# Kernel tuning notes

Hardware: AMD Instinct MI355X
Metric: run time of the kernel (lower is better)

Reference implementation:

```python
import jax, jax.numpy as jnp
import numpy as np

INPLANES = 768
HIDDEN = 64
NUM_EXPERTS = 6
TOP_K = 2


def setup_inputs() -> dict:
    key = jax.random.key(0)
    ks = jax.random.split(key, 7)
    B, C, D = 64, 320, INPLANES
    x = jax.random.normal(ks[0], (B, C, D), dtype=jnp.float32)
    xi = jax.random.normal(ks[1], (B, C, D), dtype=jnp.float32)
    # gating network: per-token logits over experts
    w_gate = jax.random.normal(ks[2], (D, NUM_EXPERTS), dtype=jnp.float32) / np.sqrt(D)
    # LoRA-style experts: down-projection D -> HIDDEN per expert
    expert_w = jax.random.normal(ks[3], (NUM_EXPERTS, D, HIDDEN), dtype=jnp.float32) / np.sqrt(D)
    expert_b = jnp.zeros((NUM_EXPERTS, HIDDEN), dtype=jnp.float32)
    # reprojection ffn1_1: Linear(HIDDEN, INPLANES), torch convention W:[out,in]
    ffn1_w = jax.random.normal(ks[4], (D, HIDDEN), dtype=jnp.float32) / np.sqrt(HIDDEN)
    ffn1_b = jnp.zeros((D,), dtype=jnp.float32)
    return {"x": x, "xi": xi, "w_gate": w_gate, "expert_w": expert_w,
            "expert_b": expert_b, "ffn1_w": ffn1_w, "ffn1_b": ffn1_b}


def _cv_squared(v):
    eps = 1e-10
    return jnp.var(v) / (jnp.mean(v) ** 2 + eps)


def reference(x, xi, w_gate, expert_w, expert_b, ffn1_w, ffn1_b):
    B, C, D = x.shape
    nz = C // 5
    # slice template (z) and search (x) token streams from both modalities
    z0, x0 = x[:, :nz, :], x[:, nz:, :]
    z1, x1 = xi[:, :nz, :], xi[:, nz:, :]
    # MoE_lora: fuse the two modalities and route tokens (z tokens first, then x)
    inp = jnp.concatenate([z0 + z1, x0 + x1], axis=1)        # [B, C, D]
    tok = inp.reshape(-1, D)                                  # [N, D], N = B*C
    N = tok.shape[0]
    # noisy-top-k gating (clean/eval path): top-2 experts, softmax over kept logits
    logits = tok @ w_gate                                     # [N, E]
    top_vals, top_idx = jax.lax.top_k(logits, TOP_K)          # [N, k]
    top_gates = jax.nn.softmax(top_vals, axis=-1)             # [N, k]
    gates = jnp.zeros_like(logits).at[jnp.arange(N)[:, None], top_idx].add(top_gates)
    # expert LoRA down-projections, combined by sparse gates (dense-equivalent math)
    h = jnp.einsum('nd,edh->enh', tok, expert_w) + expert_b[:, None, :]  # [E, N, H]
    y = jnp.einsum('ne,enh->nh', gates, h)                    # [N, H]
    y = y.reshape(B, C, HIDDEN)
    z_moe, x_moe = y[:, :nz, :], y[:, nz:, :]
    # load-balancing loss: cv^2 of importance + cv^2 of load
    importance = gates.sum(axis=0)
    load = (gates > 0).astype(jnp.float32).sum(axis=0)
    loss = _cv_squared(importance) + _cv_squared(load)
    # ffn1_1 reprojection back to inplanes
    x_prompted = x_moe @ ffn1_w.T + ffn1_b                    # [B, 4C/5, D]
    z_prompted = z_moe @ ffn1_w.T + ffn1_b                    # [B, C/5, D]
    return (x_prompted, z_prompted, loss, logits)
```

## Files before the change

### kernel.cpp

```cpp
#include <hip/hip_runtime.h>

typedef __attribute__((ext_vector_type(8))) short short8;
typedef __attribute__((ext_vector_type(4))) short short4v;
typedef __attribute__((ext_vector_type(4))) float f32x4;

#define VM(n) asm volatile("s_waitcnt vmcnt(" #n ")" ::: "memory")
#define LGKM0 asm volatile("s_waitcnt lgkmcnt(0)" ::: "memory")

namespace {

constexpr int DIN  = 768;
constexpr int HID  = 64;
constexpr int NEXP = 6;
constexpr int CDIM  = 320;
constexpr int NZ    = 64;
constexpr int NTOK  = 20480;

constexpr long long XP_OFF   = 0;
constexpr long long ZP_OFF   = 12582912LL;
constexpr long long LOSS_OFF = 15728640LL;
constexpr long long LG_OFF   = 15728641LL;

__device__ inline unsigned short f2bf(float f) {
  union { float f; unsigned u; } v{f};
  return (unsigned short)((v.u + 0x7FFFu + ((v.u >> 16) & 1u)) >> 16);
}
__device__ inline float b2f(unsigned short s) {
  union { unsigned u; float f; } v{(unsigned)s << 16};
  return v.f;
}
__device__ inline void gload16(const void* g, void* l) {
  __builtin_amdgcn_global_load_lds(
      (const __attribute__((address_space(1))) unsigned*)g,
      (__attribute__((address_space(3))) unsigned*)l, 16, 0, 0);
}
__device__ inline int row_base(int n) {
  int bb = n / CDIM, c = n - bb * CDIM;
  return (c < NZ) ? (int)(ZP_OFF + (long long)(bb * NZ + c) * DIN)
                  : (int)(XP_OFF + (long long)(bb * (CDIM - NZ) + (c - NZ)) * DIN);
}

__global__ __launch_bounds__(256) void pre_kernel(
    const float* __restrict__ x, const float* __restrict__ xi,
    const float* __restrict__ wg, const float* __restrict__ ew,
    const float* __restrict__ fw,
    float* __restrict__ out, float4* __restrict__ rec,
    unsigned short* __restrict__ ewb_t, unsigned short* __restrict__ fwb)
{
  int b = blockIdx.x, tid = threadIdx.x;
  __shared__ float t_lds[64][65];
  if (b < 72) {
    int e = b / 12, kc = (b % 12) * 64;
    const float* src = ew + (size_t)e * DIN * HID + (size_t)kc * HID;
    #pragma unroll
    for (int it = 0; it < 16; ++it) {
      int f = it * 256 + tid; int ky = f >> 6, h = f & 63;
      t_lds[h][ky] = src[ky * 64 + h];
    }
    __syncthreads();
    unsigned short* dst = ewb_t + (size_t)e * DIN * HID + kc;
    #pragma unroll
    for (int it = 0; it < 16; ++it) {
      int f = it * 256 + tid; int h = f >> 6, ky = f & 63;
      dst[(size_t)h * DIN + ky] = f2bf(t_lds[h][ky]);
    }
    return;
  }
  if (b < 84) {
    int base = (b - 72) * 4096;
    #pragma unroll
    for (int it = 0; it < 16; ++it) {
      int idx = base + it * 256 + tid;
      fwb[idx] = f2bf(fw[idx]);
    }
    return;
  }
  int wid = tid >> 6, lane = tid & 63;
  int n = (b - 84) * 4 + wid;
  float lg[NEXP];
  #pragma unroll
  for (int e = 0; e < NEXP; ++e) lg[e] = 0.f;

  const float4* xv  = reinterpret_cast<const float4*>(x  + (size_t)n * DIN);
  const float4* xiv = reinterpret_cast<const float4*>(xi + (size_t)n * DIN);
  unsigned short* tk = (unsigned short*)out + (size_t)row_base(n) * 2;
  #pragma unroll
  for (int j = 0; j < 3; ++j) {
    int f = lane + 64 * j;
    float4 a = xv[f], bq = xiv[f];
    float t0 = a.x + bq.x, t1 = a.y + bq.y, t2 = a.z + bq.z, t3 = a.w + bq.w;
    short4v tv;
    tv[0] = (short)f2bf(t0); tv[1] = (short)f2bf(t1);
    tv[2] = (short)f2bf(t2); tv[3] = (short)f2bf(t3);
    *(short4v*)(tk + f * 4) = tv;
    int d = f * 4;
    #pragma unroll
    for (int e = 0; e < NEXP; ++e) {
      lg[e] += t0 * wg[(d + 0) * NEXP + e] + t1 * wg[(d + 1) * NEXP + e]
             + t2 * wg[(d + 2) * NEXP + e] + t3 * wg[(d + 3) * NEXP + e];
    }
  }
  #pragma unroll
  for (int e = 0; e < NEXP; ++e) {
    float v = lg[e];
    #pragma unroll
    for (int off = 32; off >= 1; off >>= 1) v += __shfl_xor(v, off, 64);
    lg[e] = v;
  }
  int e0 = 0; float v0 = lg[0];
  #pragma unroll
  for (int j = 1; j < NEXP; ++j) if (lg[j] > v0) { v0 = lg[j]; e0 = j; }
  int e1 = 0; float v1 = -3.4e38f;
  #pragma unroll
  for (int j = 0; j < NEXP; ++j) if (j != e0 && lg[j] > v1) { v1 = lg[j]; e1 = j; }
  float g0 = 1.f / (1.f + expf(v1 - v0));
  if (lane < NEXP) {
    float myv = lg[0];
    #pragma unroll
    for (int e = 1; e < NEXP; ++e) if (lane == e) myv = lg[e];
    out[LG_OFF + (size_t)n * NEXP + lane] = myv;
  }
  if (lane == 0) rec[n] = make_float4((float)e0, (float)e1, g0, 1.f - g0);
}

__global__ __launch_bounds__(512) void moe_kernel(
    const unsigned short* __restrict__ ewb_t, const float* __restrict__ eb,
    const unsigned short* __restrict__ fwb, const float* __restrict__ fb,
    const float4* __restrict__ rec, float* __restrict__ out)
{
  __shared__ __align__(16) char smem[74752];
  __shared__ int rb[64];
  __shared__ float simp[8][NEXP], sld[8][NEXP];

  int tid = threadIdx.x, lane = tid & 63, wid = tid >> 6;
  int qw = lane >> 4, l15 = lane & 15;
  int wm = wid >> 2, wn = wid & 3;

  if (blockIdx.x == 320) {
    float imp[NEXP], ld[NEXP];
    #pragma unroll
    for (int e = 0; e < NEXP; ++e) { imp[e] = 0.f; ld[e] = 0.f; }
    for (int n = tid; n < NTOK; n += 512) {
      float4 r = rec[n];
      int e0 = (int)r.x, e1 = (int)r.y;
      #pragma unroll
      for (int e = 0; e < NEXP; ++e) {
        imp[e] += (e == e0 ? r.z : 0.f) + (e == e1 ? r.w : 0.f);
        ld[e]  += (e == e0 ? 1.f : 0.f) + (e == e1 ? 1.f : 0.f);
      }
    }
    #pragma unroll
    for (int e = 0; e < NEXP; ++e) {
      float a = imp[e], bq = ld[e];
      #pragma unroll
      for (int off = 32; off >= 1; off >>= 1) {
        a += __shfl_xor(a, off, 64);
        bq += __shfl_xor(bq, off, 64);
      }
      imp[e] = a; ld[e] = bq;
    }
    if (lane == 0) {
      #pragma unroll
      for (int e = 0; e < NEXP; ++e) { simp[wid][e] = imp[e]; sld[wid][e] = ld[e]; }
    }
    __syncthreads();
    if (tid == 0) {
      float It[NEXP], Lt[NEXP], mi = 0.f, ml = 0.f;
      #pragma unroll
      for (int e = 0; e < NEXP; ++e) {
        It[e] = 0.f; Lt[e] = 0.f;
        #pragma unroll
        for (int w = 0; w < 8; ++w) { It[e] += simp[w][e]; Lt[e] += sld[w][e]; }
        mi += It[e]; ml += Lt[e];
      }
      mi /= NEXP; ml /= NEXP;
      float vi = 0.f, vl = 0.f;
      #pragma unroll
      for (int e = 0; e < NEXP; ++e) {
        vi += (It[e] - mi) * (It[e] - mi);
        vl += (Lt[e] - ml) * (Lt[e] - ml);
      }
      vi /= NEXP; vl /= NEXP;
      out[LOSS_OFF] = vi / (mi * mi + 1e-10f) + vl / (ml * ml + 1e-10f);
    }
    return;
  }

  int t0 = blockIdx.x * 64;
  const unsigned short* tokb = (const unsigned short*)out;

  size_t b_src[3]; int b_dst[3];
  #pragma unroll
  for (int it = 0; it < 3; ++it) {
    int F = it * 512 + tid, r = F >> 2, s = F & 3;
    b_src[it] = (size_t)r * DIN + ((s ^ (r & 3) ^ ((r & 4) >> 1)) << 3);
    b_dst[it] = (it * 512 + wid * 64) * 16;
  }
  int ar = tid >> 2, as = tid & 3;
  size_t a_src = (size_t)row_base(t0 + ar) * 2 +
                 ((as ^ (ar & 3) ^ ((ar & 4) >> 1)) << 3);
  int a_dst = (wid * 64) * 16;

  if (tid < 64) rb[tid] = row_base(t0 + tid);

  #pragma unroll
  for (int it = 0; it < 3; ++it)
    gload16(ewb_t + b_src[it], smem + 8192 + b_dst[it]);
  if (tid < 256) gload16(tokb + a_src, smem + a_dst);

  f32x4 acc[2][6];
  #pragma unroll
  for (int m = 0; m < 2; ++m)
    #pragma unroll
    for (int n = 0; n < 6; ++n) acc[m][n] = (f32x4){0.f, 0.f, 0.f, 0.f};

  int aoff[2], boff[6];
  #pragma unroll
  for (int m = 0; m < 2; ++m) {
    int row = wm * 32 + m * 16 + l15;
    aoff[m] = row * 64 + ((qw ^ (row & 3) ^ ((row & 4) >> 1)) << 4);
  }
  #pragma unroll
  for (int n = 0; n < 6; ++n) {
    int row = wn * 96 + n * 16 + l15;
    boff[n] = row * 64 + ((qw ^ (row & 3) ^ ((row & 4) >> 1)) << 4);
  }

  for (int k = 0; k < 24; ++k) {
    const char* cA = smem + (k & 1) * 4096;
    const char* cB = smem + 8192 + (k & 1) * 24576;
    char* nA = (char*)smem + ((k + 1) & 1) * 4096;
    char* nB = (char*)smem + 8192 + ((k + 1) & 1) * 24576;
    if (k < 23) {
      #pragma unroll
      for (int it = 0; it < 3; ++it)
        gload16(ewb_t + b_src[it] + (k + 1) * 32, nB + b_dst[it]);
      if (tid < 256) gload16(tokb + a_src + (k + 1) * 32, nA + a_dst);
      if (wid < 4) VM(4); else VM(3);
    } else {
      VM(0);
    }
    __builtin_amdgcn_s_barrier();
    __builtin_amdgcn_sched_barrier(0);
    short8 af[2], bfv[6];
    #pragma unroll
    for (int m = 0; m < 2; ++m) af[m] = *(const short8*)(cA + aoff[m]);
    #pragma unroll
    for (int n = 0; n < 6; ++n) bfv[n] = *(const short8*)(cB + boff[n]);
    __builtin_amdgcn_s_setprio(1);
    #pragma unroll
    for (int m = 0; m < 2; ++m)
      #pragma unroll
      for (int n = 0; n < 6; ++n)
        acc[m][n] = __builtin_amdgcn_mfma_f32_16x16x32_bf16(af[m], bfv[n], acc[m][n], 0, 0, 0);
    __builtin_amdgcn_s_setprio(0);
    __builtin_amdgcn_sched_barrier(0);
    __builtin_amdgcn_s_barrier();
  }

  #pragma unroll
  for (int it = 0; it < 2; ++it) {
    int F = it * 512 + tid, r = F >> 3, s = F & 7;
    gload16(fwb + (size_t)r * HID + ((s ^ (r & 7)) << 3),
            smem + 58368 + (it * 512 + wid * 64) * 16);
  }

  unsigned short* hl = (unsigned short*)(smem + 8192);
  #pragma unroll
  for (int m = 0; m < 2; ++m)
    #pragma unroll
    for (int n = 0; n < 6; ++n)
      #pragma unroll
      for (int i = 0; i < 4; ++i) {
        int row = wm * 32 + m * 16 + qw * 4 + i;
        int col = wn * 96 + n * 16 + l15;
        hl[row * 392 + col] = f2bf(acc[m][n][i]);
      }
  LGKM0;
  __builtin_amdgcn_s_barrier();

  {
    int t = tid >> 3, j0 = (tid & 7) * 8;
    float4 rr = rec[t0 + t];
    int e0 = (int)rr.x, e1 = (int)rr.y;
    float g0 = rr.z, g1 = rr.w;
    short8 h0 = *(const short8*)(hl + t * 392 + e0 * 64 + j0);
    short8 h1 = *(const short8*)(hl + t * 392 + e1 * 64 + j0);
    const float4* ep0 = (const float4*)(eb + e0 * 64 + j0);
    const float4* ep1 = (const float4*)(eb + e1 * 64 + j0);
    float4 b0a = ep0[0], b0b = ep0[1], b1a = ep1[0], b1b = ep1[1];
    float be0[8] = {b0a.x, b0a.y, b0a.z, b0a.w, b0b.x, b0b.y, b0b.z, b0b.w};
    float be1[8] = {b1a.x, b1a.y, b1a.z, b1a.w, b1b.x, b1b.y, b1b.z, b1b.w};
    short8 ov;
    #pragma unroll
    for (int j = 0; j < 8; ++j) {
      float v = g0 * (b2f((unsigned short)h0[j]) + be0[j])
              + g1 * (b2f((unsigned short)h1[j]) + be1[j]);
      ov[j] = (short)f2bf(v);
    }
    *(short8*)(smem + t * 128 + ((((tid & 7)) ^ (t & 7)) << 4)) = ov;
  }
  LGKM0;
  __builtin_amdgcn_s_barrier();

  for (int c = 0; c < 6; ++c) {
    const char* cF = smem + ((c & 1) ? 8192 : 58368);
    char* nF = (char*)smem + ((c & 1) ? 58368 : 8192);
    if (c < 5) {
      #pragma unroll
      for (int it = 0; it < 2; ++it) {
        int F = it * 512 + tid, r = F >> 3, s = F & 7;
        gload16(fwb + (size_t)((c + 1) * 128 + r) * HID + ((s ^ (r & 7)) << 3),
                nF + (it * 512 + wid * 64) * 16);
      }
      VM(2);
    } else {
      VM(0);
    }
    __builtin_amdgcn_s_barrier();
    __builtin_amdgcn_sched_barrier(0);
    f32x4 a2[2][2];
    #pragma unroll
    for (int m = 0; m < 2; ++m)
      #pragma unroll
      for (int n = 0; n < 2; ++n) a2[m][n] = (f32x4){0.f, 0.f, 0.f, 0.f};
    #pragma unroll
    for (int kk = 0; kk < 2; ++kk) {
      short8 ay[2], bw[2];
      #pragma unroll
      for (int m = 0; m < 2; ++m) {
        int row = wm * 32 + m * 16 + l15;
        ay[m] = *(const short8*)(smem + row * 128 + (((kk * 4 + qw) ^ (row & 7)) << 4));
      }
      #pragma unroll
      for (int n = 0; n < 2; ++n) {
        int rw = wn * 32 + n * 16 + l15;
        bw[n] = *(const short8*)(cF + rw * 128 + (((kk * 4 + qw) ^ (rw & 7)) << 4));
      }
      __builtin_amdgcn_s_setprio(1);
      #pragma unroll
      for (int m = 0; m < 2; ++m)
        #pragma unroll
        for (int n = 0; n < 2; ++n)
          a2[m][n] = __builtin_amdgcn_mfma_f32_16x16x32_bf16(ay[m], bw[n], a2[m][n], 0, 0, 0);
      __builtin_amdgcn_s_setprio(0);
    }
    #pragma unroll
    for (int n = 0; n < 2; ++n) {
      int col = c * 128 + wn * 32 + n * 16 + l15;
      float bias = fb[col];
      #pragma unroll
      for (int m = 0; m < 2; ++m)
        #pragma unroll
        for (int i = 0; i < 4; ++i) {
          int rl = wm * 32 + m * 16 + qw * 4 + i;
          out[(size_t)rb[rl] + col] = a2[m][n][i] + bias;
        }
    }
    __builtin_amdgcn_sched_barrier(0);
    __builtin_amdgcn_s_barrier();
  }
}

}

extern "C" void kernel_launch(void* const* d_in, const int* in_sizes, int n_in,
                              void* d_out, int out_size, void* d_ws, size_t ws_size,
                              hipStream_t stream)
{
  const float* x  = (const float*)d_in[0];
  const float* xi = (const float*)d_in[1];
  const float* wg = (const float*)d_in[2];
  const float* ew = (const float*)d_in[3];
  const float* eb = (const float*)d_in[4];
  const float* fw = (const float*)d_in[5];
  const float* fb = (const float*)d_in[6];
  float* out = (float*)d_out;

  char* w = (char*)d_ws;
  float4*         rec   = (float4*)w;
  unsigned short* ewb_t = (unsigned short*)(w + 327680);
  unsigned short* fwb   = (unsigned short*)(w + 327680 + 589824);

  pre_kernel<<<84 + NTOK / 4, 256, 0, stream>>>(x, xi, wg, ew, fw, out, rec, ewb_t, fwb);
  moe_kernel<<<321, 512, 0, stream>>>(ewb_t, eb, fwb, fb, rec, out);
}
```

Measured before the change: 69.83 us.

## Process one token per 8 lanes in gating pre-kernel with LDS-staged gate weights

```diff
diff --git a/kernel.cpp b/kernel.cpp
--- a/kernel.cpp
+++ b/kernel.cpp
@@ -48,8 +48,9 @@
     unsigned short* __restrict__ ewb_t, unsigned short* __restrict__ fwb)
 {
   int b = blockIdx.x, tid = threadIdx.x;
-  __shared__ float t_lds[64][65];
+  __shared__ __align__(16) char sbuf[18432];
   if (b < 72) {
+    float (*t_lds)[65] = (float(*)[65])sbuf;
     int e = b / 12, kc = (b % 12) * 64;
     const float* src = ew + (size_t)e * DIN * HID + (size_t)kc * HID;
     #pragma unroll
@@ -75,36 +76,52 @@
     }
     return;
   }
-  int wid = tid >> 6, lane = tid & 63;
-  int n = (b - 84) * 4 + wid;
+  float* wgl = (float*)sbuf;
+  {
+    const float4* src4 = (const float4*)wg;
+    float4* dst4 = (float4*)sbuf;
+    for (int i = tid; i < NEXP * DIN / 4; i += 256) dst4[i] = src4[i];
+  }
+  __syncthreads();
+
+  int lane = tid & 63, wid = tid >> 6;
+  int ls = lane & 7;
+  int n  = (b - 84) * 32 + wid * 8 + (lane >> 3);
+
+  const float4* xv  = reinterpret_cast<const float4*>(x  + (size_t)n * DIN);
+  const float4* iv  = reinterpret_cast<const float4*>(xi + (size_t)n * DIN);
+  unsigned short* tk = (unsigned short*)out + (size_t)row_base(n) * 2;
+
   float lg[NEXP];
   #pragma unroll
   for (int e = 0; e < NEXP; ++e) lg[e] = 0.f;
 
-  const float4* xv  = reinterpret_cast<const float4*>(x  + (size_t)n * DIN);
-  const float4* xiv = reinterpret_cast<const float4*>(xi + (size_t)n * DIN);
-  unsigned short* tk = (unsigned short*)out + (size_t)row_base(n) * 2;
-  #pragma unroll
-  for (int j = 0; j < 3; ++j) {
-    int f = lane + 64 * j;
-    float4 a = xv[f], bq = xiv[f];
-    float t0 = a.x + bq.x, t1 = a.y + bq.y, t2 = a.z + bq.z, t3 = a.w + bq.w;
-    short4v tv;
-    tv[0] = (short)f2bf(t0); tv[1] = (short)f2bf(t1);
-    tv[2] = (short)f2bf(t2); tv[3] = (short)f2bf(t3);
-    *(short4v*)(tk + f * 4) = tv;
-    int d = f * 4;
-    #pragma unroll
-    for (int e = 0; e < NEXP; ++e) {
-      lg[e] += t0 * wg[(d + 0) * NEXP + e] + t1 * wg[(d + 1) * NEXP + e]
-             + t2 * wg[(d + 2) * NEXP + e] + t3 * wg[(d + 3) * NEXP + e];
-    }
+  #pragma unroll 4
+  for (int k = 0; k < 24; ++k) {
+    float4 a = xv[ls + 8 * k];
+    float4 q = iv[ls + 8 * k];
+    float tv0 = a.x + q.x, tv1 = a.y + q.y, tv2 = a.z + q.z, tv3 = a.w + q.w;
+    short4v t4;
+    t4[0] = (short)f2bf(tv0); t4[1] = (short)f2bf(tv1);
+    t4[2] = (short)f2bf(tv2); t4[3] = (short)f2bf(tv3);
+    *(short4v*)(tk + ls * 4 + 32 * k) = t4;
+    const float4* wq = (const float4*)(wgl + ls * 24 + 192 * k);
+    float4 w0 = wq[0], w1 = wq[1], w2 = wq[2], w3 = wq[3], w4 = wq[4], w5 = wq[5];
+    lg[0] += tv0 * w0.x; lg[1] += tv0 * w0.y; lg[2] += tv0 * w0.z;
+    lg[3] += tv0 * w0.w; lg[4] += tv0 * w1.x; lg[5] += tv0 * w1.y;
+    lg[0] += tv1 * w1.z; lg[1] += tv1 * w1.w; lg[2] += tv1 * w2.x;
+    lg[3] += tv1 * w2.y; lg[4] += tv1 * w2.z; lg[5] += tv1 * w2.w;
+    lg[0] += tv2 * w3.x; lg[1] += tv2 * w3.y; lg[2] += tv2 * w3.z;
+    lg[3] += tv2 * w3.w; lg[4] += tv2 * w4.x; lg[5] += tv2 * w4.y;
+    lg[0] += tv3 * w4.z; lg[1] += tv3 * w4.w; lg[2] += tv3 * w5.x;
+    lg[3] += tv3 * w5.y; lg[4] += tv3 * w5.z; lg[5] += tv3 * w5.w;
   }
   #pragma unroll
   for (int e = 0; e < NEXP; ++e) {
     float v = lg[e];
-    #pragma unroll
-    for (int off = 32; off >= 1; off >>= 1) v += __shfl_xor(v, off, 64);
+    v += __shfl_xor(v, 1, 64);
+    v += __shfl_xor(v, 2, 64);
+    v += __shfl_xor(v, 4, 64);
     lg[e] = v;
   }
   int e0 = 0; float v0 = lg[0];
@@ -114,13 +131,13 @@
   #pragma unroll
   for (int j = 0; j < NEXP; ++j) if (j != e0 && lg[j] > v1) { v1 = lg[j]; e1 = j; }
   float g0 = 1.f / (1.f + expf(v1 - v0));
-  if (lane < NEXP) {
+  if (ls < NEXP) {
     float myv = lg[0];
     #pragma unroll
-    for (int e = 1; e < NEXP; ++e) if (lane == e) myv = lg[e];
-    out[LG_OFF + (size_t)n * NEXP + lane] = myv;
-  }
-  if (lane == 0) rec[n] = make_float4((float)e0, (float)e1, g0, 1.f - g0);
+    for (int e = 1; e < NEXP; ++e) if (ls == e) myv = lg[e];
+    out[LG_OFF + (size_t)n * NEXP + ls] = myv;
+  }
+  if (ls == 0) rec[n] = make_float4((float)e0, (float)e1, g0, 1.f - g0);
 }
 
 __global__ __launch_bounds__(512) void moe_kernel(
@@ -382,6 +399,6 @@
   unsigned short* ewb_t = (unsigned short*)(w + 327680);
   unsigned short* fwb   = (unsigned short*)(w + 327680 + 589824);
 
-  pre_kernel<<<84 + NTOK / 4, 256, 0, stream>>>(x, xi, wg, ew, fw, out, rec, ewb_t, fwb);
+  pre_kernel<<<84 + 640, 256, 0, stream>>>(x, xi, wg, ew, fw, out, rec, ewb_t, fwb);
   moe_kernel<<<321, 512, 0, stream>>>(ewb_t, eb, fwb, fb, rec, out);
 }
```

Result: no change. 68.69 us (-1.6%).

## Split weight prep into separate kernel and stage token rows via LDS

Applied to the files above, without the earlier changes.

```diff
diff --git a/kernel.cpp b/kernel.cpp
--- a/kernel.cpp
+++ b/kernel.cpp
@@ -40,12 +40,11 @@
                   : (int)(XP_OFF + (long long)(bb * (CDIM - NZ) + (c - NZ)) * DIN);
 }
 
-__global__ __launch_bounds__(256) void pre_kernel(
-    const float* __restrict__ x, const float* __restrict__ xi,
-    const float* __restrict__ wg, const float* __restrict__ ew,
-    const float* __restrict__ fw,
-    float* __restrict__ out, float4* __restrict__ rec,
-    unsigned short* __restrict__ ewb_t, unsigned short* __restrict__ fwb)
+__global__ __launch_bounds__(256) void prep_kernel(
+    const float* __restrict__ ew, const float* __restrict__ fw,
+    const float* __restrict__ wg,
+    unsigned short* __restrict__ ewb_t, unsigned short* __restrict__ fwb,
+    float* __restrict__ wgT)
 {
   int b = blockIdx.x, tid = threadIdx.x;
   __shared__ float t_lds[64][65];
@@ -64,40 +63,68 @@
       int f = it * 256 + tid; int h = f >> 6, ky = f & 63;
       dst[(size_t)h * DIN + ky] = f2bf(t_lds[h][ky]);
     }
-    return;
-  }
-  if (b < 84) {
+  } else if (b < 84) {
     int base = (b - 72) * 4096;
     #pragma unroll
     for (int it = 0; it < 16; ++it) {
       int idx = base + it * 256 + tid;
       fwb[idx] = f2bf(fw[idx]);
     }
-    return;
-  }
-  int wid = tid >> 6, lane = tid & 63;
-  int n = (b - 84) * 4 + wid;
+  } else {
+    for (int idx = tid; idx < NEXP * DIN; idx += 256) {
+      int e = idx / DIN, d = idx - e * DIN;
+      wgT[idx] = wg[d * NEXP + e];
+    }
+  }
+}
+
+__global__ __launch_bounds__(512) void pre_kernel(
+    const float* __restrict__ x, const float* __restrict__ xi,
+    const float* __restrict__ wgT_g,
+    float* __restrict__ out, float4* __restrict__ rec)
+{
+  __shared__ __align__(16) char sbuf[67584];
+  int tid = threadIdx.x, lane = tid & 63, w = tid >> 6;
+  int t0 = blockIdx.x * 8;
+  char* xl = sbuf;
+  char* il = sbuf + 24576;
+  const float* wgl = (const float*)(sbuf + 49152);
+
+  #pragma unroll
+  for (int it = 0; it < 3; ++it) {
+    int s = it * 512 + tid;
+    gload16(x  + (size_t)t0 * DIN + s * 4, xl + s * 16);
+    gload16(xi + (size_t)t0 * DIN + s * 4, il + s * 16);
+  }
+  #pragma unroll
+  for (int it = 0; it < 3; ++it) {
+    int s = it * 512 + tid;
+    if (s < NEXP * DIN / 4) gload16(wgT_g + s * 4, sbuf + 49152 + s * 16);
+  }
+  VM(0);
+  __builtin_amdgcn_s_barrier();
+
+  int n = t0 + w;
+  unsigned short* tk = (unsigned short*)out + (size_t)row_base(n) * 2;
+
   float lg[NEXP];
   #pragma unroll
   for (int e = 0; e < NEXP; ++e) lg[e] = 0.f;
 
-  const float4* xv  = reinterpret_cast<const float4*>(x  + (size_t)n * DIN);
-  const float4* xiv = reinterpret_cast<const float4*>(xi + (size_t)n * DIN);
-  unsigned short* tk = (unsigned short*)out + (size_t)row_base(n) * 2;
   #pragma unroll
   for (int j = 0; j < 3; ++j) {
-    int f = lane + 64 * j;
-    float4 a = xv[f], bq = xiv[f];
-    float t0 = a.x + bq.x, t1 = a.y + bq.y, t2 = a.z + bq.z, t3 = a.w + bq.w;
-    short4v tv;
-    tv[0] = (short)f2bf(t0); tv[1] = (short)f2bf(t1);
-    tv[2] = (short)f2bf(t2); tv[3] = (short)f2bf(t3);
-    *(short4v*)(tk + f * 4) = tv;
-    int d = f * 4;
+    int d = lane * 4 + 256 * j;
+    float4 a = *(const float4*)(xl + w * 3072 + d * 4);
+    float4 q = *(const float4*)(il + w * 3072 + d * 4);
+    float tv0 = a.x + q.x, tv1 = a.y + q.y, tv2 = a.z + q.z, tv3 = a.w + q.w;
+    short4v t4;
+    t4[0] = (short)f2bf(tv0); t4[1] = (short)f2bf(tv1);
+    t4[2] = (short)f2bf(tv2); t4[3] = (short)f2bf(tv3);
+    *(short4v*)(tk + d) = t4;
     #pragma unroll
     for (int e = 0; e < NEXP; ++e) {
-      lg[e] += t0 * wg[(d + 0) * NEXP + e] + t1 * wg[(d + 1) * NEXP + e]
-             + t2 * wg[(d + 2) * NEXP + e] + t3 * wg[(d + 3) * NEXP + e];
+      float4 wv = *(const float4*)(wgl + e * DIN + d);
+      lg[e] += tv0 * wv.x + tv1 * wv.y + tv2 * wv.z + tv3 * wv.w;
     }
   }
   #pragma unroll
@@ -381,7 +408,9 @@
   float4*         rec   = (float4*)w;
   unsigned short* ewb_t = (unsigned short*)(w + 327680);
   unsigned short* fwb   = (unsigned short*)(w + 327680 + 589824);
-
-  pre_kernel<<<84 + NTOK / 4, 256, 0, stream>>>(x, xi, wg, ew, fw, out, rec, ewb_t, fwb);
+  float*          wgT   = (float*)(w + 327680 + 589824 + 98304);
+
+  prep_kernel<<<85, 256, 0, stream>>>(ew, fw, wg, ewb_t, fwb, wgT);
+  pre_kernel<<<NTOK / 8, 512, 0, stream>>>(x, xi, wgT, out, rec);
   moe_kernel<<<321, 512, 0, stream>>>(ewb_t, eb, fwb, fb, rec, out);
 }
```

Measured after the change: 73.45 us. +5.2%, slower.
